# Kernel optimization log

Hardware: AMD Instinct MI355X
Metric: run time of the kernel (lower is better)

The kernel has to match this reference:

```python
import jax, jax.numpy as jnp
import numpy as np
import math

B, S, H = 2, 2048, 3072
NH, NKV, HD = 32, 32, 96
BASE = 10000.0
NEG = -1e9


def rotate_half(x):
    x1 = x[..., : x.shape[-1] // 2]
    x2 = x[..., x.shape[-1] // 2 :]
    return jnp.concatenate((-x2, x1), axis=-1)


def setup_inputs() -> dict:
    key = jax.random.key(0)
    k1, k2, k3 = jax.random.split(key, 3)
    hidden_states = jax.random.normal(k1, (B, S, H), dtype=jnp.float32)
    position_ids = jnp.broadcast_to(jnp.arange(S, dtype=jnp.int32), (B, S))
    # additive causal mask: 0 where key <= query, -1e9 above the diagonal
    i = jnp.arange(S)
    causal = jnp.where(i[None, :] <= i[:, None], 0.0, NEG).astype(jnp.float32)
    attention_mask = jnp.broadcast_to(causal[None, None], (B, 1, S, S))
    w_qkv = jax.random.normal(k2, (NH * HD + 2 * NKV * HD, H), dtype=jnp.float32) * 0.02
    w_o = jax.random.normal(k3, (H, NH * HD), dtype=jnp.float32) * 0.02
    return {
        "hidden_states": hidden_states,
        "position_ids": position_ids,
        "attention_mask": attention_mask,
        "w_qkv": w_qkv,
        "w_o": w_o,
    }


def reference(hidden_states, position_ids, attention_mask, w_qkv, w_o):
    bsz, q_len, _ = hidden_states.shape
    # fused QKV projection (no bias), then split per Phi3 layout
    qkv = jnp.einsum("bsh,oh->bso", hidden_states, w_qkv)
    q = qkv[..., : NH * HD]
    k = qkv[..., NH * HD : NH * HD + NKV * HD]
    v = qkv[..., NH * HD + NKV * HD :]
    q = q.reshape(bsz, q_len, NH, HD).transpose(0, 2, 1, 3)   # [B,NH,S,HD]
    k = k.reshape(bsz, q_len, NKV, HD).transpose(0, 2, 1, 3)  # [B,NKV,S,HD]
    v = v.reshape(bsz, q_len, NKV, HD).transpose(0, 2, 1, 3)

    # rotary embeddings (Phi3RotaryEmbedding, no scaling)
    inv_freq = 1.0 / (BASE ** (jnp.arange(0, HD, 2, dtype=jnp.float32) / HD))  # [HD/2]
    freqs = position_ids.astype(jnp.float32)[:, :, None] * inv_freq[None, None, :]  # [B,S,HD/2]
    emb = jnp.concatenate((freqs, freqs), axis=-1)  # [B,S,HD]
    cos = jnp.cos(emb)[:, None].astype(hidden_states.dtype)  # [B,1,S,HD]
    sin = jnp.sin(emb)[:, None].astype(hidden_states.dtype)
    q = q * cos + rotate_half(q) * sin
    k = k * cos + rotate_half(k) * sin
    # num_key_value_groups = NH // NKV = 1 -> repeat_kv is a no-op

    attn = jnp.einsum("bhqd,bhkd->bhqk", q, k) / math.sqrt(HD)
    attn = attn + attention_mask  # broadcast over heads
    attn = jax.nn.softmax(attn.astype(jnp.float32), axis=-1).astype(v.dtype)
    # attention_dropout = 0.0 / eval mode -> dropout is identity
    out = jnp.einsum("bhqk,bhkd->bhqd", attn, v)
    out = out.transpose(0, 2, 1, 3).reshape(bsz, q_len, NH * HD)
    return jnp.einsum("bso,ho->bsh", out, w_o)
```

## Files before the change

kernel.cpp:

```cpp
#include <hip/hip_runtime.h>
#include <hip/hip_bf16.h>
#include <type_traits>

typedef unsigned short ushort_t;
typedef __attribute__((ext_vector_type(8))) short bf16x8;
typedef __attribute__((ext_vector_type(4))) float f32x4;

#define S_LEN 2048
#define NHEAD 32
#define HDIM 96

__device__ __forceinline__ float bf2f(ushort_t b) {
    union { unsigned u; float f; } v; v.u = ((unsigned)b) << 16; return v.f;
}
__device__ __forceinline__ ushort_t f2bf(float f) {
    union { float f; unsigned u; } v; v.f = f;
    unsigned r = v.u + 0x7fffu + ((v.u >> 16) & 1u);
    return (ushort_t)(r >> 16);
}
__device__ __forceinline__ void cp16(ushort_t* l, const ushort_t* g) {
    __builtin_amdgcn_global_load_lds((const __attribute__((address_space(1))) void*)g,
                                     (__attribute__((address_space(3))) void*)l, 16, 0, 0);
}

__global__ void cvt_f32_bf16(const float* __restrict__ src, ushort_t* __restrict__ dst, int n8)
{
    const int i = blockIdx.x * 256 + threadIdx.x;
    if (i >= n8) return;
    const float4 a = ((const float4*)src)[2 * i];
    const float4 b = ((const float4*)src)[2 * i + 1];
    union { ushort_t us[8]; int4 v; } r;
    r.us[0] = f2bf(a.x); r.us[1] = f2bf(a.y); r.us[2] = f2bf(a.z); r.us[3] = f2bf(a.w);
    r.us[4] = f2bf(b.x); r.us[5] = f2bf(b.y); r.us[6] = f2bf(b.z); r.us[7] = f2bf(b.w);
    ((int4*)dst)[i] = r.v;
}

__global__ __launch_bounds__(768, 3) void gemm288(
    const ushort_t* __restrict__ A, const ushort_t* __restrict__ Bm,
    ushort_t* __restrict__ C, int M, int N, int K)
{
    __shared__ ushort_t As[2][16384];
    __shared__ ushort_t Bs[2][18432];
    const int tid = threadIdx.x;
    const int lane = tid & 63, w = tid >> 6;
    const int wm = w / 6, wn = w % 6;
    const int r16 = lane & 15, quad = lane >> 4;

    const int m0 = blockIdx.y * 256;
    const int n0 = blockIdx.x * 288;

    const ushort_t* gp[3];
    ushort_t* lp[3];
    int bstr[3], pstr[3];
#pragma unroll
    for (int j = 0; j < 3; j++) {
        int c = tid + 768 * j;
        if (c >= 2176) c -= 2176;
        if (c < 1024) {
            const int row = c >> 2;
            gp[j] = A + (size_t)(m0 + row) * K + (((c & 3) ^ ((row >> 1) & 3)) * 8);
            lp[j] = &As[0][c * 8];
            bstr[j] = 16384; pstr[j] = 8192;
        } else {
            const int cb = c - 1024;
            const int row = cb >> 2;
            gp[j] = Bm + (size_t)(n0 + row) * K + (((cb & 3) ^ ((row >> 1) & 3)) * 8);
            lp[j] = &Bs[0][cb * 8];
            bstr[j] = 18432; pstr[j] = 9216;
        }
    }
#define STAGE(buf, ks, ko) { \
    cp16(lp[0] + (buf) * bstr[0] + (ks) * pstr[0], gp[0] + (ko) + (ks) * 32); \
    cp16(lp[1] + (buf) * bstr[1] + (ks) * pstr[1], gp[1] + (ko) + (ks) * 32); \
    cp16(lp[2] + (buf) * bstr[2] + (ks) * pstr[2], gp[2] + (ko) + (ks) * 32); }

    const int laneoff = r16 * 32 + (quad ^ ((r16 >> 1) & 3)) * 8;

    f32x4 acc[8][3];
#pragma unroll
    for (int m = 0; m < 8; m++)
#pragma unroll
        for (int j = 0; j < 3; j++) acc[m][j] = f32x4{0.f, 0.f, 0.f, 0.f};

    const int NT = K >> 6;

    STAGE(0, 0, 0);
    STAGE(0, 1, 0);
    asm volatile("s_waitcnt vmcnt(3)" ::: "memory");
    __builtin_amdgcn_s_barrier();
    asm volatile("" ::: "memory");

    for (int t = 0; t < NT; ++t) {
        const int b = t & 1, bn = b ^ 1;
        const int ko = (t + 1) << 6;
        bf16x8 av[8], bv[3];

#pragma unroll
        for (int j = 0; j < 3; j++)
            bv[j] = *(const bf16x8*)&Bs[b][(wn * 48 + j * 16) * 32 + laneoff];
#pragma unroll
        for (int m = 0; m < 8; m++)
            av[m] = *(const bf16x8*)&As[b][(wm * 128 + m * 16) * 32 + laneoff];
        if (t + 1 < NT) STAGE(bn, 0, ko);
        __builtin_amdgcn_s_barrier();
        asm volatile("" ::: "memory");
        __builtin_amdgcn_s_setprio(1);
#pragma unroll
        for (int m = 0; m < 8; m++)
#pragma unroll
            for (int j = 0; j < 3; j++)
                acc[m][j] = __builtin_amdgcn_mfma_f32_16x16x32_bf16(av[m], bv[j], acc[m][j], 0, 0, 0);
        __builtin_amdgcn_s_setprio(0);
        if (t + 1 < NT) {
            asm volatile("s_waitcnt vmcnt(3)" ::: "memory");
        } else {
            asm volatile("s_waitcnt vmcnt(0)" ::: "memory");
        }
        __builtin_amdgcn_s_barrier();
        asm volatile("" ::: "memory");

#pragma unroll
        for (int j = 0; j < 3; j++)
            bv[j] = *(const bf16x8*)&Bs[b][9216 + (wn * 48 + j * 16) * 32 + laneoff];
#pragma unroll
        for (int m = 0; m < 8; m++)
            av[m] = *(const bf16x8*)&As[b][8192 + (wm * 128 + m * 16) * 32 + laneoff];
        if (t + 1 < NT) STAGE(bn, 1, ko);
        __builtin_amdgcn_s_barrier();
        asm volatile("" ::: "memory");
        __builtin_amdgcn_s_setprio(1);
#pragma unroll
        for (int m = 0; m < 8; m++)
#pragma unroll
            for (int j = 0; j < 3; j++)
                acc[m][j] = __builtin_amdgcn_mfma_f32_16x16x32_bf16(av[m], bv[j], acc[m][j], 0, 0, 0);
        __builtin_amdgcn_s_setprio(0);
        if (t + 1 < NT) {
            asm volatile("s_waitcnt vmcnt(3)" ::: "memory");
        } else {
            asm volatile("s_waitcnt vmcnt(0)" ::: "memory");
        }
        __builtin_amdgcn_s_barrier();
        asm volatile("" ::: "memory");
    }
#undef STAGE

#pragma unroll
    for (int m = 0; m < 8; m++) {
        const int row0 = m0 + wm * 128 + m * 16 + quad * 4;
#pragma unroll
        for (int j = 0; j < 3; j++) {
            const int col = n0 + wn * 48 + j * 16 + r16;
#pragma unroll
            for (int r = 0; r < 4; r++)
                C[(size_t)(row0 + r) * N + col] = f2bf(acc[m][j][r]);
        }
    }
}

template <typename OT>
__global__ __launch_bounds__(512, 2) void gemm256(
    const ushort_t* __restrict__ A, const ushort_t* __restrict__ Bm,
    OT* __restrict__ C, int M, int N, int K)
{
    __shared__ ushort_t As[2][16384];
    __shared__ ushort_t Bs[2][12288];
    const int tid = threadIdx.x;
    const int lane = tid & 63, w = tid >> 6;
    const int wm = w >> 2, wn = w & 3;
    const int r16 = lane & 15, quad = lane >> 4;

    const int m0 = blockIdx.y * 256;
    const int n0 = blockIdx.x * 192;

    const int sl8 = ((tid & 3) ^ ((tid >> 3) & 3)) * 8;
    const int srow = tid >> 2;
    const ushort_t* gA  = A  + (size_t)(m0 + srow) * K + sl8;
    const size_t rsk = (size_t)128 * K;
    const ushort_t* gB0 = Bm + (size_t)(n0 + srow) * K + sl8;
    const ushort_t* gB1 = Bm + (size_t)(n0 + ((tid < 256) ? (128 + srow) : ((tid - 256) >> 2))) * K
                          + ((tid < 256) ? 0 : 32) + sl8;
    const ushort_t* gB2 = Bm + (size_t)(n0 + 64 + srow) * K + 32 + sl8;

    const int laneoff = r16 * 32 + (quad ^ ((r16 >> 1) & 3)) * 8;

    f32x4 acc[8][3];
#pragma unroll
    for (int m = 0; m < 8; m++)
#pragma unroll
        for (int j = 0; j < 3; j++) acc[m][j] = f32x4{0.f, 0.f, 0.f, 0.f};

    const int NT = K >> 6;

#define STAGE_B(bn, kb)  { cp16(&Bs[bn][tid * 8],         gB0 + (kb)); \
                           cp16(&Bs[bn][tid * 8 + 4096],  gB1 + (kb)); \
                           cp16(&Bs[bn][tid * 8 + 8192],  gB2 + (kb)); }
#define STAGE_A0(bn, kb) { cp16(&As[bn][tid * 8],         gA + (kb)); \
                           cp16(&As[bn][tid * 8 + 4096],  gA + rsk + (kb)); }
#define STAGE_A1(bn, kb) { cp16(&As[bn][tid * 8 + 8192],  gA + (kb) + 32); \
                           cp16(&As[bn][tid * 8 + 12288], gA + rsk + (kb) + 32); }

    STAGE_B(0, 0);
    STAGE_A0(0, 0);
    STAGE_A1(0, 0);
    asm volatile("s_waitcnt vmcnt(2)" ::: "memory");
    __builtin_amdgcn_s_barrier();

    for (int t = 0; t < NT; ++t) {
        const int b = t & 1, bn = b ^ 1;
        const int kb = (t + 1) << 6;
        bf16x8 av[8], bv[3];

#pragma unroll
        for (int j = 0; j < 3; j++)
            bv[j] = *(const bf16x8*)&Bs[b][(wn * 48 + j * 16) * 32 + laneoff];
#pragma unroll
        for (int m = 0; m < 8; m++)
            av[m] = *(const bf16x8*)&As[b][(wm * 128 + m * 16) * 32 + laneoff];
        if (t + 1 < NT) {
            STAGE_B(bn, kb);
            STAGE_A0(bn, kb);
        }
        __builtin_amdgcn_s_barrier();
        __builtin_amdgcn_s_setprio(1);
#pragma unroll
        for (int m = 0; m < 8; m++)
#pragma unroll
            for (int j = 0; j < 3; j++)
                acc[m][j] = __builtin_amdgcn_mfma_f32_16x16x32_bf16(av[m], bv[j], acc[m][j], 0, 0, 0);
        __builtin_amdgcn_s_setprio(0);
        if (t + 1 < NT) {
            asm volatile("s_waitcnt vmcnt(5)" ::: "memory");
        } else {
            asm volatile("s_waitcnt vmcnt(0)" ::: "memory");
        }
        __builtin_amdgcn_s_barrier();

#pragma unroll
        for (int j = 0; j < 3; j++)
            bv[j] = *(const bf16x8*)&Bs[b][6144 + (wn * 48 + j * 16) * 32 + laneoff];
#pragma unroll
        for (int m = 0; m < 8; m++)
            av[m] = *(const bf16x8*)&As[b][8192 + (wm * 128 + m * 16) * 32 + laneoff];
        if (t + 1 < NT) {
            STAGE_A1(bn, kb);
        }
        __builtin_amdgcn_s_barrier();
        __builtin_amdgcn_s_setprio(1);
#pragma unroll
        for (int m = 0; m < 8; m++)
#pragma unroll
            for (int j = 0; j < 3; j++)
                acc[m][j] = __builtin_amdgcn_mfma_f32_16x16x32_bf16(av[m], bv[j], acc[m][j], 0, 0, 0);
        __builtin_amdgcn_s_setprio(0);
        asm volatile("s_waitcnt vmcnt(2)" ::: "memory");
        __builtin_amdgcn_s_barrier();
    }
#undef STAGE_B
#undef STAGE_A0
#undef STAGE_A1

#pragma unroll
    for (int m = 0; m < 8; m++) {
        const int row0 = m0 + wm * 128 + m * 16 + quad * 4;
#pragma unroll
        for (int j = 0; j < 3; j++) {
            const int col = n0 + wn * 48 + j * 16 + r16;
#pragma unroll
            for (int r = 0; r < 4; r++) {
                if constexpr (std::is_same<OT, float>::value)
                    C[(size_t)(row0 + r) * N + col] = acc[m][j][r];
                else
                    C[(size_t)(row0 + r) * N + col] = f2bf(acc[m][j][r]);
            }
        }
    }
}

__global__ void rope_scatter(const ushort_t* __restrict__ qkv, const int* __restrict__ pos,
                             ushort_t* __restrict__ Q, ushort_t* __restrict__ Kd)
{
    const int d = threadIdx.x;
    const int t = blockIdx.x * 2 + threadIdx.y;
    const int h = blockIdx.y;
    const int which = d >= 48;
    const int dd = which ? d - 48 : d;
    const int p = pos[t];
    const float inv = exp2f((float)dd * (-13.287712379549449f / 48.0f));
    const float th = (float)p * inv;
    const float cs = cosf(th), sn = sinf(th);
    const ushort_t* src = qkv + (size_t)t * 9216 + (which ? 3072 : 0) + h * 96;
    const float x1 = bf2f(src[dd]), x2 = bf2f(src[dd + 48]);
    ushort_t* dst = (which ? Kd : Q) +
        ((size_t)((t >> 11) * NHEAD + h) * S_LEN + (t & 2047)) * HDIM;
    dst[dd]      = f2bf(x1 * cs - x2 * sn);
    dst[dd + 48] = f2bf(x2 * cs + x1 * sn);
}

__global__ __launch_bounds__(256) void v_transpose2(const ushort_t* __restrict__ qkv,
                                                    ushort_t* __restrict__ VT)
{
    __shared__ ushort_t tl[64 * 102];
    const int tid = threadIdx.x;
    const int s0 = blockIdx.x * 64;
    const int h  = blockIdx.y;
    const int b  = blockIdx.z;
    const ushort_t* src = qkv + ((size_t)(b * 2048 + s0)) * 9216 + 6144 + h * 96;
#pragma unroll
    for (int k = 0; k < 24; k++) {
        const int idx = tid + 256 * k;
        const int r = idx / 96, c = idx % 96;
        tl[r * 102 + c] = src[(size_t)r * 9216 + c];
    }
    __syncthreads();
    ushort_t* dst = VT + (size_t)(b * NHEAD + h) * HDIM * S_LEN + s0;
#pragma unroll
    for (int k = 0; k < 24; k++) {
        const int idx = tid + 256 * k;
        const int d = idx >> 6, s = idx & 63;
        dst[(size_t)d * S_LEN + s] = tl[s * 102 + d];
    }
}

__global__ __launch_bounds__(256, 2) void flash_attn(
    const ushort_t* __restrict__ Q, const ushort_t* __restrict__ Kg,
    const ushort_t* __restrict__ VT, ushort_t* __restrict__ attn)
{
    __shared__ ushort_t Qs[128 * 104];
    __shared__ ushort_t Ps[128 * 72];

    const int tid = threadIdx.x, w = tid >> 6, lane = tid & 63;
    const int r16 = lane & 15, quad = lane >> 4;
    const int qi = 15 - (blockIdx.x >> 6);
    const int bh = blockIdx.x & 63;
    const int q0 = qi * 128;
    const ushort_t* Qg  = Q  + ((size_t)bh * S_LEN + q0) * HDIM;
    const ushort_t* Kgb = Kg + (size_t)bh * S_LEN * HDIM;
    const ushort_t* Vgb = VT + (size_t)bh * HDIM * S_LEN;

#pragma unroll
    for (int c = 0; c < 6; c++) {
        const int cc = tid + 256 * c;
        const int row = cc / 12, col = (cc % 12) * 8;
        *(int4*)&Qs[row * 104 + col] = *(const int4*)(Qg + row * 96 + col);
    }
    __syncthreads();

    float m_st[2][4], l_st[2][4];
#pragma unroll
    for (int i = 0; i < 2; i++)
#pragma unroll
        for (int r = 0; r < 4; r++) { m_st[i][r] = -1.0e30f; l_st[i][r] = 0.f; }

    f32x4 o[2][6];
#pragma unroll
    for (int i = 0; i < 2; i++)
#pragma unroll
        for (int jo = 0; jo < 6; jo++) o[i][jo] = f32x4{0.f, 0.f, 0.f, 0.f};

    const float sc = 0.10206207261596577f;
    const float L2E = 1.4426950408889634f;
    const int nkt = 2 * qi + 2;
    const int rowb = 32 * w;

    for (int kt = 0; kt < nkt; ++kt) {
        const int k0 = kt * 64;

        f32x4 sacc[2][4];
#pragma unroll
        for (int i = 0; i < 2; i++)
#pragma unroll
            for (int j = 0; j < 4; j++) sacc[i][j] = f32x4{0.f, 0.f, 0.f, 0.f};
#pragma unroll
        for (int kk = 0; kk < 3; kk++) {
            bf16x8 qa[2], kb[4];
#pragma unroll
            for (int i = 0; i < 2; i++)
                qa[i] = *(const bf16x8*)&Qs[(rowb + 16 * i + r16) * 104 + kk * 32 + quad * 8];
#pragma unroll
            for (int j = 0; j < 4; j++)
                kb[j] = *(const bf16x8*)(Kgb + (size_t)(k0 + 16 * j + r16) * 96
                                         + kk * 32 + quad * 8);
#pragma unroll
            for (int i = 0; i < 2; i++)
#pragma unroll
                for (int j = 0; j < 4; j++)
                    sacc[i][j] = __builtin_amdgcn_mfma_f32_16x16x32_bf16(qa[i], kb[j], sacc[i][j], 0, 0, 0);
        }

        const bool need_mask = (kt >= 2 * qi);
#pragma unroll
        for (int i = 0; i < 2; i++)
#pragma unroll
            for (int j = 0; j < 4; j++)
#pragma unroll
                for (int r = 0; r < 4; r++) {
                    float v = sacc[i][j][r] * sc;
                    if (need_mask) {
                        const int grow = q0 + rowb + 16 * i + quad * 4 + r;
                        const int gcol = k0 + 16 * j + r16;
                        if (gcol > grow) v = -1.0e9f;
                    }
                    sacc[i][j][r] = v;
                }

        float mt[2][4];
#pragma unroll
        for (int i = 0; i < 2; i++)
#pragma unroll
            for (int r = 0; r < 4; r++) {
                float mp = fmaxf(fmaxf(sacc[i][0][r], sacc[i][1][r]),
                                 fmaxf(sacc[i][2][r], sacc[i][3][r]));
                mp = fmaxf(mp, __shfl_xor(mp, 1, 16));
                mp = fmaxf(mp, __shfl_xor(mp, 2, 16));
                mp = fmaxf(mp, __shfl_xor(mp, 4, 16));
                mp = fmaxf(mp, __shfl_xor(mp, 8, 16));
                mt[i][r] = mp;
            }

        float alpha[2][4];
#pragma unroll
        for (int i = 0; i < 2; i++)
#pragma unroll
            for (int r = 0; r < 4; r++) {
                const float mn = fmaxf(m_st[i][r], mt[i][r]);
                alpha[i][r] = exp2f((m_st[i][r] - mn) * L2E);
                m_st[i][r] = mn;
            }

        float psum[2][4];
#pragma unroll
        for (int i = 0; i < 2; i++)
#pragma unroll
            for (int r = 0; r < 4; r++) psum[i][r] = 0.f;
#pragma unroll
        for (int i = 0; i < 2; i++)
#pragma unroll
            for (int j = 0; j < 4; j++)
#pragma unroll
                for (int r = 0; r < 4; r++) {
                    const float p = exp2f((sacc[i][j][r] - m_st[i][r]) * L2E);
                    psum[i][r] += p;
                    Ps[(rowb + 16 * i + quad * 4 + r) * 72 + 16 * j + r16] = f2bf(p);
                }
#pragma unroll
        for (int i = 0; i < 2; i++)
#pragma unroll
            for (int r = 0; r < 4; r++) {
                float s2 = psum[i][r];
                s2 += __shfl_xor(s2, 1, 16);
                s2 += __shfl_xor(s2, 2, 16);
                s2 += __shfl_xor(s2, 4, 16);
                s2 += __shfl_xor(s2, 8, 16);
                l_st[i][r] = l_st[i][r] * alpha[i][r] + s2;
            }

#pragma unroll
        for (int i = 0; i < 2; i++)
#pragma unroll
            for (int jo = 0; jo < 6; jo++)
#pragma unroll
                for (int r = 0; r < 4; r++) o[i][jo][r] *= alpha[i][r];
#pragma unroll
        for (int kk = 0; kk < 2; kk++) {
            bf16x8 pa[2], vb[6];
#pragma unroll
            for (int i = 0; i < 2; i++)
                pa[i] = *(const bf16x8*)&Ps[(rowb + 16 * i + r16) * 72 + kk * 32 + quad * 8];
#pragma unroll
            for (int jo = 0; jo < 6; jo++)
                vb[jo] = *(const bf16x8*)(Vgb + (size_t)(16 * jo + r16) * S_LEN
                                          + k0 + kk * 32 + quad * 8);
#pragma unroll
            for (int i = 0; i < 2; i++)
#pragma unroll
                for (int jo = 0; jo < 6; jo++)
                    o[i][jo] = __builtin_amdgcn_mfma_f32_16x16x32_bf16(pa[i], vb[jo], o[i][jo], 0, 0, 0);
        }
    }

    const int b = bh >> 5, h = bh & 31;
#pragma unroll
    for (int i = 0; i < 2; i++)
#pragma unroll
        for (int r = 0; r < 4; r++) {
            const int lr = rowb + 16 * i + quad * 4 + r;
            const float inv = 1.0f / l_st[i][r];
            const size_t base = (size_t)(b * S_LEN + q0 + lr) * 3072 + h * 96;
#pragma unroll
            for (int jo = 0; jo < 6; jo++)
                attn[base + 16 * jo + r16] = f2bf(o[i][jo][r] * inv);
        }
}

extern "C" void kernel_launch(void* const* d_in, const int* in_sizes, int n_in,
                              void* d_out, int out_size, void* d_ws, size_t ws_size,
                              hipStream_t stream)
{
    const float* hidden = (const float*)d_in[0];
    const int*   pos    = (const int*)d_in[1];
    const float* w_qkv  = (const float*)d_in[3];
    const float* w_o    = (const float*)d_in[4];
    float* out          = (float*)d_out;

    char* ws = (char*)d_ws;
    ushort_t* hbf    = (ushort_t*)(ws);
    ushort_t* wqkvbf = (ushort_t*)(ws + 25165824);
    ushort_t* Qb     = (ushort_t*)(ws);
    ushort_t* Kb     = (ushort_t*)(ws + 25165824);
    ushort_t* VTb    = (ushort_t*)(ws + 50331648);
    ushort_t* qkv    = (ushort_t*)(ws + 81788928);
    ushort_t* attn   = qkv;
    ushort_t* wobf   = (ushort_t*)(ws + 157286400);

    cvt_f32_bf16<<<dim3(12582912 / 8 / 256), 256, 0, stream>>>(hidden, hbf, 12582912 / 8);
    cvt_f32_bf16<<<dim3(28311552 / 8 / 256), 256, 0, stream>>>(w_qkv, wqkvbf, 28311552 / 8);
    cvt_f32_bf16<<<dim3(9437184 / 8 / 256), 256, 0, stream>>>(w_o, wobf, 9437184 / 8);

    gemm288<<<dim3(32, 16), 768, 0, stream>>>(hbf, wqkvbf, qkv, 4096, 9216, 3072);
    rope_scatter<<<dim3(2048, 32), dim3(96, 2), 0, stream>>>(qkv, pos, Qb, Kb);
    v_transpose2<<<dim3(32, 32, 2), 256, 0, stream>>>(qkv, VTb);
    flash_attn<<<dim3(1024), 256, 0, stream>>>(Qb, Kb, VTb, attn);
    gemm256<float><<<dim3(16, 16), 512, 0, stream>>>(attn, wobf, out, 4096, 3072, 3072);
}
```

Before: 737.5 us.

## Merge GEMM k-substage barriers, add lazy softmax rescaling, raise attention occupancy

The GEMM main loop now issues both half-tile prefetches at once and keeps one wait and one barrier per iteration instead of four barriers, cutting synchronisation overhead at the cost of a less fine-grained overlap. The flash-attention kernel folds the score scale and log2e into one FMA constant, masks with a large negative value only on diagonal tiles, and skips rescaling of the running max, sum and output when no row's max grows by more than a threshold. Launch bounds move to three blocks per SM, which pressures registers and may cause spills. Lazy rescaling lets the un-normalised exponentials grow up to a bounded factor, which relies on fp32 and bf16 range being large enough.

Result: slower. 771.3 us (+4.6%).

```diff
diff --git a/kernel.cpp b/kernel.cpp
--- a/kernel.cpp
+++ b/kernel.cpp
@@ -86,7 +86,7 @@
 
     STAGE(0, 0, 0);
     STAGE(0, 1, 0);
-    asm volatile("s_waitcnt vmcnt(3)" ::: "memory");
+    asm volatile("s_waitcnt vmcnt(0)" ::: "memory");
     __builtin_amdgcn_s_barrier();
     asm volatile("" ::: "memory");
 
@@ -101,9 +101,7 @@
 #pragma unroll
         for (int m = 0; m < 8; m++)
             av[m] = *(const bf16x8*)&As[b][(wm * 128 + m * 16) * 32 + laneoff];
-        if (t + 1 < NT) STAGE(bn, 0, ko);
-        __builtin_amdgcn_s_barrier();
-        asm volatile("" ::: "memory");
+        if (t + 1 < NT) { STAGE(bn, 0, ko); STAGE(bn, 1, ko); }
         __builtin_amdgcn_s_setprio(1);
 #pragma unroll
         for (int m = 0; m < 8; m++)
@@ -111,23 +109,12 @@
             for (int j = 0; j < 3; j++)
                 acc[m][j] = __builtin_amdgcn_mfma_f32_16x16x32_bf16(av[m], bv[j], acc[m][j], 0, 0, 0);
         __builtin_amdgcn_s_setprio(0);
-        if (t + 1 < NT) {
-            asm volatile("s_waitcnt vmcnt(3)" ::: "memory");
-        } else {
-            asm volatile("s_waitcnt vmcnt(0)" ::: "memory");
-        }
-        __builtin_amdgcn_s_barrier();
-        asm volatile("" ::: "memory");
-
 #pragma unroll
         for (int j = 0; j < 3; j++)
             bv[j] = *(const bf16x8*)&Bs[b][9216 + (wn * 48 + j * 16) * 32 + laneoff];
 #pragma unroll
         for (int m = 0; m < 8; m++)
             av[m] = *(const bf16x8*)&As[b][8192 + (wm * 128 + m * 16) * 32 + laneoff];
-        if (t + 1 < NT) STAGE(bn, 1, ko);
-        __builtin_amdgcn_s_barrier();
-        asm volatile("" ::: "memory");
         __builtin_amdgcn_s_setprio(1);
 #pragma unroll
         for (int m = 0; m < 8; m++)
@@ -135,11 +122,7 @@
             for (int j = 0; j < 3; j++)
                 acc[m][j] = __builtin_amdgcn_mfma_f32_16x16x32_bf16(av[m], bv[j], acc[m][j], 0, 0, 0);
         __builtin_amdgcn_s_setprio(0);
-        if (t + 1 < NT) {
-            asm volatile("s_waitcnt vmcnt(3)" ::: "memory");
-        } else {
-            asm volatile("s_waitcnt vmcnt(0)" ::: "memory");
-        }
+        asm volatile("s_waitcnt vmcnt(0)" ::: "memory");
         __builtin_amdgcn_s_barrier();
         asm volatile("" ::: "memory");
     }
@@ -322,7 +305,7 @@
     }
 }
 
-__global__ __launch_bounds__(256, 2) void flash_attn(
+__global__ __launch_bounds__(256, 3) void flash_attn(
     const ushort_t* __restrict__ Q, const ushort_t* __restrict__ Kg,
     const ushort_t* __restrict__ VT, ushort_t* __restrict__ attn)
 {
@@ -358,8 +341,8 @@
 #pragma unroll
         for (int jo = 0; jo < 6; jo++) o[i][jo] = f32x4{0.f, 0.f, 0.f, 0.f};
 
-    const float sc = 0.10206207261596577f;
-    const float L2E = 1.4426950408889634f;
+    const float CS  = 0.14724920020342437f;
+    const float RTH = 54.329f;
     const int nkt = 2 * qi + 2;
     const int rowb = 32 * w;
 
@@ -388,21 +371,18 @@
                     sacc[i][j] = __builtin_amdgcn_mfma_f32_16x16x32_bf16(qa[i], kb[j], sacc[i][j], 0, 0, 0);
         }
 
-        const bool need_mask = (kt >= 2 * qi);
-#pragma unroll
-        for (int i = 0; i < 2; i++)
-#pragma unroll
-            for (int j = 0; j < 4; j++)
-#pragma unroll
-                for (int r = 0; r < 4; r++) {
-                    float v = sacc[i][j][r] * sc;
-                    if (need_mask) {
+        if (kt >= 2 * qi) {
+#pragma unroll
+            for (int i = 0; i < 2; i++)
+#pragma unroll
+                for (int j = 0; j < 4; j++)
+#pragma unroll
+                    for (int r = 0; r < 4; r++) {
                         const int grow = q0 + rowb + 16 * i + quad * 4 + r;
                         const int gcol = k0 + 16 * j + r16;
-                        if (gcol > grow) v = -1.0e9f;
+                        if (gcol > grow) sacc[i][j][r] = -3.0e38f;
                     }
-                    sacc[i][j][r] = v;
-                }
+        }
 
         float mt[2][4];
 #pragma unroll
@@ -418,16 +398,36 @@
                 mt[i][r] = mp;
             }
 
-        float alpha[2][4];
-#pragma unroll
-        for (int i = 0; i < 2; i++)
-#pragma unroll
-            for (int r = 0; r < 4; r++) {
-                const float mn = fmaxf(m_st[i][r], mt[i][r]);
-                alpha[i][r] = exp2f((m_st[i][r] - mn) * L2E);
-                m_st[i][r] = mn;
-            }
-
+        int okl = 1;
+#pragma unroll
+        for (int i = 0; i < 2; i++)
+#pragma unroll
+            for (int r = 0; r < 4; r++)
+                okl &= (mt[i][r] - m_st[i][r] <= RTH) ? 1 : 0;
+        if (!__all(okl)) {
+            float alpha[2][4];
+#pragma unroll
+            for (int i = 0; i < 2; i++)
+#pragma unroll
+                for (int r = 0; r < 4; r++) {
+                    const float mn = fmaxf(m_st[i][r], mt[i][r]);
+                    alpha[i][r] = exp2f((m_st[i][r] - mn) * CS);
+                    m_st[i][r] = mn;
+                    l_st[i][r] *= alpha[i][r];
+                }
+#pragma unroll
+            for (int i = 0; i < 2; i++)
+#pragma unroll
+                for (int jo = 0; jo < 6; jo++)
+#pragma unroll
+                    for (int r = 0; r < 4; r++) o[i][jo][r] *= alpha[i][r];
+        }
+
+        float nmcs[2][4];
+#pragma unroll
+        for (int i = 0; i < 2; i++)
+#pragma unroll
+            for (int r = 0; r < 4; r++) nmcs[i][r] = -m_st[i][r] * CS;
         float psum[2][4];
 #pragma unroll
         for (int i = 0; i < 2; i++)
@@ -439,7 +439,7 @@
             for (int j = 0; j < 4; j++)
 #pragma unroll
                 for (int r = 0; r < 4; r++) {
-                    const float p = exp2f((sacc[i][j][r] - m_st[i][r]) * L2E);
+                    const float p = exp2f(fmaf(sacc[i][j][r], CS, nmcs[i][r]));
                     psum[i][r] += p;
                     Ps[(rowb + 16 * i + quad * 4 + r) * 72 + 16 * j + r16] = f2bf(p);
                 }
@@ -452,15 +452,9 @@
                 s2 += __shfl_xor(s2, 2, 16);
                 s2 += __shfl_xor(s2, 4, 16);
                 s2 += __shfl_xor(s2, 8, 16);
-                l_st[i][r] = l_st[i][r] * alpha[i][r] + s2;
+                l_st[i][r] += s2;
             }
 
-#pragma unroll
-        for (int i = 0; i < 2; i++)
-#pragma unroll
-            for (int jo = 0; jo < 6; jo++)
-#pragma unroll
-                for (int r = 0; r < 4; r++) o[i][jo][r] *= alpha[i][r];
 #pragma unroll
         for (int kk = 0; kk < 2; kk++) {
             bf16x8 pa[2], vb[6];
```
